# Kernel tuning notes

Measured on AMD Instinct MI355X. Metric: run time of the kernel, lower is better.

The kernel has to match this reference:

```python
import jax, jax.numpy as jnp
import numpy as np

B, IN_E, IN_I, D = 4096, 4096, 4096, 2048
IN_BR = 8192
BS = IN_BR // D  # block size = 4
K_E, K_I = 50, 1
E_TO_I = 50.0
BN_EPS = 1e-5


def setup_inputs() -> dict:
    key = jax.random.key(0)
    ks = jax.random.split(key, 8)
    # fan-in uniform init like nn.Linear (kaiming-uniform bound ~ 1/sqrt(in))
    def linw(k, out_f, in_f):
        b = 1.0 / np.sqrt(in_f)
        return jax.random.uniform(k, (out_f, in_f), jnp.float32, -b, b)
    return {
        "excitatory_input": jax.random.normal(ks[0], (B, IN_E), jnp.float32),
        "inhibitory_input": jax.random.normal(ks[1], (B, IN_I), jnp.float32),
        "dendrite_branch_outputs": jax.random.uniform(ks[2], (B, IN_BR), jnp.float32),
        "w_exc": linw(ks[3], D, IN_E),
        "w_inh": linw(ks[4], D, IN_I),
        "w_block": linw(ks[5], D, IN_BR),
        "bn_gamma": jnp.ones((D,), jnp.float32),
        "bn_beta": jnp.zeros((D,), jnp.float32),
    }


def _topk_linear(x, w, k):
    # keep the k largest weights per output row, zero the rest, then matmul
    idx = jax.lax.top_k(w, k)[1]                          # [D, k]
    mask = jnp.zeros_like(w).at[jnp.arange(w.shape[0])[:, None], idx].set(1.0)
    return x @ (w * mask).T                               # [B, D]


def _block_linear(x, w):
    # block-diagonal mask: row c uses columns [c*BS, (c+1)*BS)
    out_f = w.shape[0]
    wb = w.reshape(out_f, out_f, BS)[jnp.arange(out_f), jnp.arange(out_f)]  # [D, BS]
    xb = x.reshape(x.shape[0], out_f, BS)                                   # [B, D, BS]
    return jnp.einsum('bds,ds->bd', xb, wb)


def reference(excitatory_input, inhibitory_input, dendrite_branch_outputs,
              w_exc, w_inh, w_block, bn_gamma, bn_beta):
    dendrite_excitation = _topk_linear(excitatory_input, w_exc, K_E)
    dendrite_inhibition = _topk_linear(inhibitory_input, w_inh, K_I)
    dendrite_depolarization = _block_linear(dendrite_branch_outputs, w_block)
    total_excitatory = dendrite_excitation + dendrite_depolarization
    # neuron_type == 'excitatory'
    act = total_excitatory - E_TO_I * dendrite_inhibition
    # BatchNorm1d, training mode: batch stats, biased variance
    mean = jnp.mean(act, axis=0)
    var = jnp.var(act, axis=0)
    act = (act - mean) * jax.lax.rsqrt(var + BN_EPS) * bn_gamma + bn_beta
    return jax.nn.sigmoid(act)
```

## Files before the change

### kernel.cpp

```cpp
#include <hip/hip_runtime.h>
#include <hip/hip_fp16.h>

#define B_     4096
#define INE_   4096
#define INBR_  8192
#define D_     2048
#define KE_    50
#define KPAD_  52
#define CAP_   512

__device__ __forceinline__ unsigned packh2(float a, float b) {
  __half2 h = __floats2half2_rn(a, b);
  return __builtin_bit_cast(unsigned, h);
}
__device__ __forceinline__ float2 unpackh2(unsigned u) {
  __half2 h = __builtin_bit_cast(__half2, u);
  return __half22float2(h);
}

__global__ __launch_bounds__(256) void extract_diag(
    const float* __restrict__ wblock, float* __restrict__ wdiag)
{
  int d = blockIdx.x * 256 + threadIdx.x;
  float4 w = *reinterpret_cast<const float4*>(wblock + (size_t)d * (INBR_ + 4));
  reinterpret_cast<float4*>(wdiag)[d] = w;
}

__global__ __launch_bounds__(256) void topk_kernel(
    const float* __restrict__ W, int k, int kpad, float hi, float t0,
    float vscale, unsigned* __restrict__ out_off, float* __restrict__ out_val)
{
  const int row = blockIdx.x;
  const int t   = threadIdx.x;
  const float* wr = W + (size_t)row * INE_;

  __shared__ float cval[CAP_];
  __shared__ int   ccol[CAP_];
  __shared__ int   scnt;
  __shared__ int   red[4];

  float thr = t0;
  int M = 0;
  for (int attempt = 0; attempt < 8; ++attempt) {
    int local = 0;
    #pragma unroll
    for (int j = 0; j < 4; ++j) {
      float4 w4 = *reinterpret_cast<const float4*>(wr + 4 * (t + 256 * j));
      local += (w4.x > thr) + (w4.y > thr) + (w4.z > thr) + (w4.w > thr);
    }
    #pragma unroll
    for (int off = 32; off > 0; off >>= 1) local += __shfl_down(local, off);
    if ((t & 63) == 0) red[t >> 6] = local;
    __syncthreads();
    M = red[0] + red[1] + red[2] + red[3];
    __syncthreads();
    if (M >= k && M <= CAP_) break;
    if (M < k) thr = hi - (hi - thr) * 4.0f;
    else       thr = hi - (hi - thr) * 0.5f;
  }

  if (t == 0) scnt = 0;
  __syncthreads();
  #pragma unroll
  for (int j = 0; j < 4; ++j) {
    int cbase = 4 * (t + 256 * j);
    float4 w4 = *reinterpret_cast<const float4*>(wr + cbase);
    float wv[4] = {w4.x, w4.y, w4.z, w4.w};
    #pragma unroll
    for (int q = 0; q < 4; ++q) {
      if (wv[q] > thr) {
        int p = atomicAdd(&scnt, 1);
        if (p < CAP_) { cval[p] = wv[q]; ccol[p] = cbase + q; }
      }
    }
  }
  __syncthreads();
  M = scnt < CAP_ ? scnt : CAP_;

  for (int i = t; i < M; i += 256) {
    float wi = cval[i]; int ci = ccol[i];
    int rank = 0;
    for (int m = 0; m < M; ++m) {
      float wm = cval[m]; int cm = ccol[m];
      rank += (wm > wi || (wm == wi && cm < ci)) ? 1 : 0;
    }
    if (rank < k) {
      unsigned c = (unsigned)ci;
      unsigned off = ((c >> 2) << 3) | ((c & 3u) << 13);
      float    val = wi * vscale;
      if (kpad == 1) {
        out_off[row] = off;
        out_val[row] = val;
      } else {
        size_t idx = ((size_t)(rank >> 2) * D_ + row) * 4 + (rank & 3);
        out_off[idx] = off;
        out_val[idx] = val;
      }
    }
  }
  if (kpad > 1 && t < kpad - k) {
    int slot = k + t;
    size_t idx = ((size_t)(slot >> 2) * D_ + row) * 4 + (slot & 3);
    out_off[idx] = 0u;
    out_val[idx] = 0.0f;
  }
}

__device__ __forceinline__ void stage_rows4(const float* __restrict__ src,
                                            unsigned* xs, int b0, int p, int Q) {
  const float* r0p = src + (size_t)(b0 + 2 * p)     * INE_;
  const float* r1p = src + (size_t)(b0 + 2 * p + 1) * INE_;
  #pragma unroll
  for (int m = 0; m < 4; ++m) {
    int c0 = 4 * Q + 1024 * m;
    float4 fa = *reinterpret_cast<const float4*>(r0p + c0);
    float4 fb = *reinterpret_cast<const float4*>(r1p + c0);
    int wb = 2 * (Q + 256 * m) + p;
    xs[wb]        = packh2(fa.x, fb.x);
    xs[wb + 2048] = packh2(fa.y, fb.y);
    xs[wb + 4096] = packh2(fa.z, fb.z);
    xs[wb + 6144] = packh2(fa.w, fb.w);
  }
}

__device__ __forceinline__ uint2 ldg2(const char* ldsb, unsigned off) {
  return *reinterpret_cast<const uint2*>(ldsb + off);
}

#define FMA4(R, G, WV) do {                                                \
    float2 f0 = unpackh2((G).x), f1 = unpackh2((G).y);                     \
    acc[R][0] = fmaf(f0.x, (WV), acc[R][0]);                               \
    acc[R][1] = fmaf(f0.y, (WV), acc[R][1]);                               \
    acc[R][2] = fmaf(f1.x, (WV), acc[R][2]);                               \
    acc[R][3] = fmaf(f1.y, (WV), acc[R][3]);                               \
  } while (0)

__global__ __launch_bounds__(512, 4) void fused_main(
    const float* __restrict__ xe, const float* __restrict__ xi,
    const float* __restrict__ xbr, const float* __restrict__ wdiag,
    const unsigned* __restrict__ soT, const float* __restrict__ veT,
    const unsigned* __restrict__ so_inh, const float* __restrict__ vi_inh,
    float* __restrict__ act)
{
  __shared__ unsigned xs[8192];
  const int t  = threadIdx.x;
  const int b0 = blockIdx.x * 4;
  const int p  = t & 1;
  const int Q  = t >> 1;

  float acc[4][4];
  #pragma unroll
  for (int r = 0; r < 4; ++r)
    #pragma unroll
    for (int b = 0; b < 4; ++b) acc[r][b] = 0.0f;

  const char* ldsb = reinterpret_cast<const char*>(xs);
  const uint4*  soT4 = reinterpret_cast<const uint4*>(soT);
  const float4* veT4 = reinterpret_cast<const float4*>(veT);

  stage_rows4(xe, xs, b0, p, Q);
  __syncthreads();
  for (int ii = 0; ii < KPAD_ / 4; ++ii) {
    uint4 o[4]; float4 v[4];
    #pragma unroll
    for (int r = 0; r < 4; ++r) {
      o[r] = soT4[ii * D_ + t + 512 * r];
      v[r] = veT4[ii * D_ + t + 512 * r];
    }
    uint2 g[4][4];
    #pragma unroll
    for (int r = 0; r < 4; ++r) {
      g[r][0] = ldg2(ldsb, o[r].x);
      g[r][1] = ldg2(ldsb, o[r].y);
      g[r][2] = ldg2(ldsb, o[r].z);
      g[r][3] = ldg2(ldsb, o[r].w);
    }
    #pragma unroll
    for (int r = 0; r < 4; ++r) {
      FMA4(r, g[r][0], v[r].x);
      FMA4(r, g[r][1], v[r].y);
      FMA4(r, g[r][2], v[r].z);
      FMA4(r, g[r][3], v[r].w);
    }
  }
  __syncthreads();

  stage_rows4(xi, xs, b0, p, Q);
  unsigned oi[4]; float vi[4];
  #pragma unroll
  for (int r = 0; r < 4; ++r) {
    const int d = t + 512 * r;
    oi[r] = so_inh[d];
    vi[r] = vi_inh[d];
  }
  __syncthreads();
  {
    uint2 gi[4];
    #pragma unroll
    for (int r = 0; r < 4; ++r) gi[r] = ldg2(ldsb, oi[r]);
    #pragma unroll
    for (int r = 0; r < 4; ++r) FMA4(r, gi[r], vi[r]);
  }

  #pragma unroll
  for (int r = 0; r < 4; ++r) {
    const int d = t + 512 * r;
    float4 wb4 = reinterpret_cast<const float4*>(wdiag)[d];
    #pragma unroll
    for (int b = 0; b < 4; ++b) {
      float4 xb4 = *reinterpret_cast<const float4*>(
          xbr + (size_t)(b0 + b) * INBR_ + 4 * d);
      acc[r][b] += xb4.x * wb4.x + xb4.y * wb4.y + xb4.z * wb4.z + xb4.w * wb4.w;
    }
  }

  #pragma unroll
  for (int r = 0; r < 4; ++r) {
    const int d = t + 512 * r;
    #pragma unroll
    for (int b = 0; b < 4; ++b)
      act[(size_t)(b0 + b) * D_ + d] = acc[r][b];
  }
}

__global__ __launch_bounds__(256) void reduce_stats(
    const float* __restrict__ act, float* __restrict__ sums,
    float* __restrict__ sumsq)
{
  const int dg = blockIdx.x & 63;
  const int rg = blockIdx.x >> 6;
  const int tx = threadIdx.x & 31;
  const int ty = threadIdx.x >> 5;
  const int d  = dg * 32 + tx;

  float s = 0.0f, s2 = 0.0f;
  #pragma unroll 4
  for (int i = 0; i < 64; ++i) {
    int row = rg * 512 + ty + 8 * i;
    float a = act[(size_t)row * D_ + d];
    s += a;
    s2 = fmaf(a, a, s2);
  }
  __shared__ float ls[2][8][32];
  ls[0][ty][tx] = s;
  ls[1][ty][tx] = s2;
  __syncthreads();
  if (ty == 0) {
    #pragma unroll
    for (int j = 1; j < 8; ++j) { s += ls[0][j][tx]; s2 += ls[1][j][tx]; }
    atomicAdd(&sums[d], s);
    atomicAdd(&sumsq[d], s2);
  }
}

__global__ __launch_bounds__(256) void finalize_stats(
    const float* __restrict__ sums, const float* __restrict__ sumsq,
    const float* __restrict__ gamma, const float* __restrict__ beta,
    float* __restrict__ scsh)
{
  int d = blockIdx.x * 256 + threadIdx.x;
  if (d < D_) {
    float mean = sums[d]  * (1.0f / B_);
    float var  = sumsq[d] * (1.0f / B_) - mean * mean;
    float rstd = rsqrtf(var + 1e-5f);
    float sc   = gamma[d] * rstd;
    scsh[2 * d]     = sc;
    scsh[2 * d + 1] = fmaf(-mean, sc, beta[d]);
  }
}

__global__ __launch_bounds__(256) void norm_sigmoid(
    float* __restrict__ act, const float* __restrict__ scsh)
{
  const int total4 = (B_ * D_) / 4;
  for (int i = blockIdx.x * blockDim.x + threadIdx.x; i < total4;
       i += gridDim.x * blockDim.x) {
    float4 a = reinterpret_cast<float4*>(act)[i];
    int d0 = (i * 4) & (D_ - 1);
    const float4* sp = reinterpret_cast<const float4*>(scsh + 2 * d0);
    float4 s0 = sp[0];
    float4 s1 = sp[1];
    float z0 = fmaf(a.x, s0.x, s0.y);
    float z1 = fmaf(a.y, s0.z, s0.w);
    float z2 = fmaf(a.z, s1.x, s1.y);
    float z3 = fmaf(a.w, s1.z, s1.w);
    a.x = 1.0f / (1.0f + __expf(-z0));
    a.y = 1.0f / (1.0f + __expf(-z1));
    a.z = 1.0f / (1.0f + __expf(-z2));
    a.w = 1.0f / (1.0f + __expf(-z3));
    reinterpret_cast<float4*>(act)[i] = a;
  }
}

extern "C" void kernel_launch(void* const* d_in, const int* in_sizes, int n_in,
                              void* d_out, int out_size, void* d_ws, size_t ws_size,
                              hipStream_t stream) {
  const float* xe    = (const float*)d_in[0];
  const float* xi    = (const float*)d_in[1];
  const float* xbr   = (const float*)d_in[2];
  const float* wexc  = (const float*)d_in[3];
  const float* winh  = (const float*)d_in[4];
  const float* wblk  = (const float*)d_in[5];
  const float* gamma = (const float*)d_in[6];
  const float* beta  = (const float*)d_in[7];
  float* act = (float*)d_out;

  char* ws = (char*)d_ws;
  unsigned* soT    = (unsigned*)(ws + 0);
  float*    veT    = (float*)   (ws + 425984);
  unsigned* so_inh = (unsigned*)(ws + 851968);
  float*    vi_inh = (float*)   (ws + 860160);
  float*    wdiag  = (float*)   (ws + 868352);
  float*    sums   = (float*)   (ws + 901120);
  float*    sumsq  = (float*)   (ws + 909312);
  float*    scsh   = (float*)   (ws + 917504);

  hipMemsetAsync(sums, 0, 2 * D_ * sizeof(float), stream);

  const float hi = 0.015625f;
  extract_diag<<<dim3(8), dim3(256), 0, stream>>>(wblk, wdiag);
  topk_kernel<<<dim3(D_), dim3(256), 0, stream>>>(
      wexc, KE_, KPAD_, hi, hi * (1.0f - 200.0f / 4096.0f), 1.0f, soT, veT);
  topk_kernel<<<dim3(D_), dim3(256), 0, stream>>>(
      winh, 1, 1, hi, hi * (1.0f - 48.0f / 4096.0f), -50.0f, so_inh, vi_inh);
  fused_main<<<dim3(B_ / 4), dim3(512), 0, stream>>>(
      xe, xi, xbr, wdiag, soT, veT, so_inh, vi_inh, act);
  reduce_stats<<<dim3(512), dim3(256), 0, stream>>>(act, sums, sumsq);
  finalize_stats<<<dim3((D_ + 255) / 256), dim3(256), 0, stream>>>(
      sums, sumsq, gamma, beta, scsh);
  norm_sigmoid<<<dim3(2048), dim3(256), 0, stream>>>(act, scsh);
}
```

Baseline: 141.4 us.

## Merge prep kernels, fuse BN stats into main kernel, overlap loads with gather

The three preprocessing kernels (diagonal extraction and the two top-k selections) are merged into one launch. The main kernel now accumulates per-feature sum and sum-of-squares with atomics into four slice buffers, which removes the separate pass that re-read the activations. Inhibitory input rows and the block-diagonal branch terms are loaded while the excitatory gather loop runs, to hide global latency. Finalize and normalize+sigmoid are combined into one tail kernel that keeps the scale/shift table in shared memory. In exchange there is more atomic traffic and higher register pressure in the main kernel.

```diff
diff --git a/kernel.cpp b/kernel.cpp
--- a/kernel.cpp
+++ b/kernel.cpp
@@ -8,6 +8,7 @@
 #define KE_    50
 #define KPAD_  52
 #define CAP_   512
+#define NSL_   4
 
 __device__ __forceinline__ unsigned packh2(float a, float b) {
   __half2 h = __floats2half2_rn(a, b);
@@ -18,20 +19,11 @@
   return __half22float2(h);
 }
 
-__global__ __launch_bounds__(256) void extract_diag(
-    const float* __restrict__ wblock, float* __restrict__ wdiag)
+__device__ void topk_body(const float* __restrict__ W, int row, int k, int kpad,
+                          float hi, float t0, float vscale,
+                          unsigned* __restrict__ out_off, float* __restrict__ out_val)
 {
-  int d = blockIdx.x * 256 + threadIdx.x;
-  float4 w = *reinterpret_cast<const float4*>(wblock + (size_t)d * (INBR_ + 4));
-  reinterpret_cast<float4*>(wdiag)[d] = w;
-}
-
-__global__ __launch_bounds__(256) void topk_kernel(
-    const float* __restrict__ W, int k, int kpad, float hi, float t0,
-    float vscale, unsigned* __restrict__ out_off, float* __restrict__ out_val)
-{
-  const int row = blockIdx.x;
-  const int t   = threadIdx.x;
+  const int t = threadIdx.x;
   const float* wr = W + (size_t)row * INE_;
 
   __shared__ float cval[CAP_];
@@ -69,8 +61,8 @@
     #pragma unroll
     for (int q = 0; q < 4; ++q) {
       if (wv[q] > thr) {
-        int p = atomicAdd(&scnt, 1);
-        if (p < CAP_) { cval[p] = wv[q]; ccol[p] = cbase + q; }
+        int pp = atomicAdd(&scnt, 1);
+        if (pp < CAP_) { cval[pp] = wv[q]; ccol[pp] = cbase + q; }
       }
     }
   }
@@ -106,6 +98,32 @@
   }
 }
 
+__global__ __launch_bounds__(256) void prep_kernel(
+    const float* __restrict__ wexc, const float* __restrict__ winh,
+    const float* __restrict__ wblk,
+    unsigned* __restrict__ soT, float* __restrict__ veT,
+    unsigned* __restrict__ so_inh, float* __restrict__ vi_inh,
+    float* __restrict__ wdiag)
+{
+  const int bid = blockIdx.x;
+  const float hi = 0.015625f;
+  if (bid < 2048) {
+    topk_body(wexc, bid, KE_, KPAD_, hi, hi * (1.0f - 200.0f / 4096.0f), 1.0f,
+              soT, veT);
+  } else if (bid < 4096) {
+    topk_body(winh, bid - 2048, 1, 1, hi, hi * (1.0f - 48.0f / 4096.0f), -50.0f,
+              so_inh, vi_inh);
+  } else {
+    const int t = threadIdx.x;
+    #pragma unroll
+    for (int j = 0; j < 8; ++j) {
+      int d = t + 256 * j;
+      float4 w = *reinterpret_cast<const float4*>(wblk + (size_t)d * (INBR_ + 4));
+      reinterpret_cast<float4*>(wdiag)[d] = w;
+    }
+  }
+}
+
 __device__ __forceinline__ void stage_rows4(const float* __restrict__ src,
                                             unsigned* xs, int b0, int p, int Q) {
   const float* r0p = src + (size_t)(b0 + 2 * p)     * INE_;
@@ -135,12 +153,49 @@
     acc[R][3] = fmaf(f1.y, (WV), acc[R][3]);                               \
   } while (0)
 
+#define GATHER_ITER(II) do {                                               \
+    uint4 o_[4]; float4 v_[4];                                             \
+    _Pragma("unroll")                                                      \
+    for (int r = 0; r < 4; ++r) {                                          \
+      o_[r] = soT4[(II) * D_ + t + 512 * r];                               \
+      v_[r] = veT4[(II) * D_ + t + 512 * r];                               \
+    }                                                                      \
+    uint2 gq_[4][4];                                                       \
+    _Pragma("unroll")                                                      \
+    for (int r = 0; r < 4; ++r) {                                          \
+      gq_[r][0] = ldg2(ldsb, o_[r].x);                                     \
+      gq_[r][1] = ldg2(ldsb, o_[r].y);                                     \
+      gq_[r][2] = ldg2(ldsb, o_[r].z);                                     \
+      gq_[r][3] = ldg2(ldsb, o_[r].w);                                     \
+    }                                                                      \
+    _Pragma("unroll")                                                      \
+    for (int r = 0; r < 4; ++r) {                                          \
+      FMA4(r, gq_[r][0], v_[r].x);                                         \
+      FMA4(r, gq_[r][1], v_[r].y);                                         \
+      FMA4(r, gq_[r][2], v_[r].z);                                         \
+      FMA4(r, gq_[r][3], v_[r].w);                                         \
+    }                                                                      \
+  } while (0)
+
+#define BR_CHUNK(R_) do {                                                  \
+    const int d_ = t + 512 * (R_);                                         \
+    float4 wb4 = reinterpret_cast<const float4*>(wdiag)[d_];               \
+    _Pragma("unroll")                                                      \
+    for (int b = 0; b < 4; ++b) {                                          \
+      float4 xb4 = *reinterpret_cast<const float4*>(                       \
+          xbr + (size_t)(b0 + b) * INBR_ + 4 * d_);                        \
+      acc[R_][b] += xb4.x * wb4.x + xb4.y * wb4.y +                        \
+                    xb4.z * wb4.z + xb4.w * wb4.w;                         \
+    }                                                                      \
+  } while (0)
+
 __global__ __launch_bounds__(512, 4) void fused_main(
     const float* __restrict__ xe, const float* __restrict__ xi,
     const float* __restrict__ xbr, const float* __restrict__ wdiag,
     const unsigned* __restrict__ soT, const float* __restrict__ veT,
     const unsigned* __restrict__ so_inh, const float* __restrict__ vi_inh,
-    float* __restrict__ act)
+    float* __restrict__ act, float* __restrict__ sums_p,
+    float* __restrict__ sumsq_p)
 {
   __shared__ unsigned xs[8192];
   const int t  = threadIdx.x;
@@ -160,135 +215,114 @@
 
   stage_rows4(xe, xs, b0, p, Q);
   __syncthreads();
-  for (int ii = 0; ii < KPAD_ / 4; ++ii) {
-    uint4 o[4]; float4 v[4];
-    #pragma unroll
-    for (int r = 0; r < 4; ++r) {
-      o[r] = soT4[ii * D_ + t + 512 * r];
-      v[r] = veT4[ii * D_ + t + 512 * r];
-    }
-    uint2 g[4][4];
-    #pragma unroll
-    for (int r = 0; r < 4; ++r) {
-      g[r][0] = ldg2(ldsb, o[r].x);
-      g[r][1] = ldg2(ldsb, o[r].y);
-      g[r][2] = ldg2(ldsb, o[r].z);
-      g[r][3] = ldg2(ldsb, o[r].w);
-    }
-    #pragma unroll
-    for (int r = 0; r < 4; ++r) {
-      FMA4(r, g[r][0], v[r].x);
-      FMA4(r, g[r][1], v[r].y);
-      FMA4(r, g[r][2], v[r].z);
-      FMA4(r, g[r][3], v[r].w);
-    }
-  }
-  __syncthreads();
-
-  stage_rows4(xi, xs, b0, p, Q);
-  unsigned oi[4]; float vi[4];
+
+  float4 xia[4], xib[4];
+  {
+    const float* xr0 = xi + (size_t)(b0 + 2 * p)     * INE_;
+    const float* xr1 = xi + (size_t)(b0 + 2 * p + 1) * INE_;
+    #pragma unroll
+    for (int m = 0; m < 4; ++m) {
+      xia[m] = *reinterpret_cast<const float4*>(xr0 + 4 * Q + 1024 * m);
+      xib[m] = *reinterpret_cast<const float4*>(xr1 + 4 * Q + 1024 * m);
+    }
+  }
+  unsigned oi[4]; float viv[4];
+  #pragma unroll
+  for (int r = 0; r < 4; ++r) {
+    oi[r]  = so_inh[t + 512 * r];
+    viv[r] = vi_inh[t + 512 * r];
+  }
+
+  #pragma unroll
+  for (int g = 0; g < 4; ++g) {
+    for (int jj = 0; jj < 3; ++jj) {
+      int ii = 3 * g + jj;
+      GATHER_ITER(ii);
+    }
+    BR_CHUNK(g);
+  }
+  GATHER_ITER(12);
+  __syncthreads();
+
+  #pragma unroll
+  for (int m = 0; m < 4; ++m) {
+    int wb = 2 * (Q + 256 * m) + p;
+    xs[wb]        = packh2(xia[m].x, xib[m].x);
+    xs[wb + 2048] = packh2(xia[m].y, xib[m].y);
+    xs[wb + 4096] = packh2(xia[m].z, xib[m].z);
+    xs[wb + 6144] = packh2(xia[m].w, xib[m].w);
+  }
+  __syncthreads();
+  {
+    uint2 gi[4];
+    #pragma unroll
+    for (int r = 0; r < 4; ++r) gi[r] = ldg2(ldsb, oi[r]);
+    #pragma unroll
+    for (int r = 0; r < 4; ++r) FMA4(r, gi[r], viv[r]);
+  }
+
+  const int slice = blockIdx.x >> 8;
   #pragma unroll
   for (int r = 0; r < 4; ++r) {
     const int d = t + 512 * r;
-    oi[r] = so_inh[d];
-    vi[r] = vi_inh[d];
-  }
-  __syncthreads();
-  {
-    uint2 gi[4];
-    #pragma unroll
-    for (int r = 0; r < 4; ++r) gi[r] = ldg2(ldsb, oi[r]);
-    #pragma unroll
-    for (int r = 0; r < 4; ++r) FMA4(r, gi[r], vi[r]);
-  }
-
-  #pragma unroll
-  for (int r = 0; r < 4; ++r) {
-    const int d = t + 512 * r;
-    float4 wb4 = reinterpret_cast<const float4*>(wdiag)[d];
+    float s = 0.0f, s2 = 0.0f;
     #pragma unroll
     for (int b = 0; b < 4; ++b) {
-      float4 xb4 = *reinterpret_cast<const float4*>(
-          xbr + (size_t)(b0 + b) * INBR_ + 4 * d);
-      acc[r][b] += xb4.x * wb4.x + xb4.y * wb4.y + xb4.z * wb4.z + xb4.w * wb4.w;
-    }
-  }
-
-  #pragma unroll
-  for (int r = 0; r < 4; ++r) {
-    const int d = t + 512 * r;
-    #pragma unroll
-    for (int b = 0; b < 4; ++b)
-      act[(size_t)(b0 + b) * D_ + d] = acc[r][b];
-  }
-}
-
-__global__ __launch_bounds__(256) void reduce_stats(
-    const float* __restrict__ act, float* __restrict__ sums,
-    float* __restrict__ sumsq)
+      float a = acc[r][b];
+      act[(size_t)(b0 + b) * D_ + d] = a;
+      s += a;
+      s2 = fmaf(a, a, s2);
+    }
+    atomicAdd(&sums_p[slice * D_ + d], s);
+    atomicAdd(&sumsq_p[slice * D_ + d], s2);
+  }
+}
+
+__global__ __launch_bounds__(256) void tail_kernel(
+    float* __restrict__ act, const float* __restrict__ sums_p,
+    const float* __restrict__ sumsq_p, const float* __restrict__ gamma,
+    const float* __restrict__ beta)
 {
-  const int dg = blockIdx.x & 63;
-  const int rg = blockIdx.x >> 6;
-  const int tx = threadIdx.x & 31;
-  const int ty = threadIdx.x >> 5;
-  const int d  = dg * 32 + tx;
-
-  float s = 0.0f, s2 = 0.0f;
-  #pragma unroll 4
-  for (int i = 0; i < 64; ++i) {
-    int row = rg * 512 + ty + 8 * i;
-    float a = act[(size_t)row * D_ + d];
-    s += a;
-    s2 = fmaf(a, a, s2);
-  }
-  __shared__ float ls[2][8][32];
-  ls[0][ty][tx] = s;
-  ls[1][ty][tx] = s2;
-  __syncthreads();
-  if (ty == 0) {
-    #pragma unroll
-    for (int j = 1; j < 8; ++j) { s += ls[0][j][tx]; s2 += ls[1][j][tx]; }
-    atomicAdd(&sums[d], s);
-    atomicAdd(&sumsq[d], s2);
-  }
-}
-
-__global__ __launch_bounds__(256) void finalize_stats(
-    const float* __restrict__ sums, const float* __restrict__ sumsq,
-    const float* __restrict__ gamma, const float* __restrict__ beta,
-    float* __restrict__ scsh)
-{
-  int d = blockIdx.x * 256 + threadIdx.x;
-  if (d < D_) {
-    float mean = sums[d]  * (1.0f / B_);
-    float var  = sumsq[d] * (1.0f / B_) - mean * mean;
+  __shared__ float scsh[2 * D_];
+  const int tid = threadIdx.x;
+  #pragma unroll
+  for (int j = 0; j < 8; ++j) {
+    int d = tid + 256 * j;
+    float s = 0.0f, s2 = 0.0f;
+    #pragma unroll
+    for (int sl = 0; sl < NSL_; ++sl) {
+      s  += sums_p[sl * D_ + d];
+      s2 += sumsq_p[sl * D_ + d];
+    }
+    float mean = s  * (1.0f / B_);
+    float var  = s2 * (1.0f / B_) - mean * mean;
     float rstd = rsqrtf(var + 1e-5f);
     float sc   = gamma[d] * rstd;
     scsh[2 * d]     = sc;
     scsh[2 * d + 1] = fmaf(-mean, sc, beta[d]);
   }
-}
-
-__global__ __launch_bounds__(256) void norm_sigmoid(
-    float* __restrict__ act, const float* __restrict__ scsh)
-{
-  const int total4 = (B_ * D_) / 4;
-  for (int i = blockIdx.x * blockDim.x + threadIdx.x; i < total4;
-       i += gridDim.x * blockDim.x) {
-    float4 a = reinterpret_cast<float4*>(act)[i];
-    int d0 = (i * 4) & (D_ - 1);
-    const float4* sp = reinterpret_cast<const float4*>(scsh + 2 * d0);
-    float4 s0 = sp[0];
-    float4 s1 = sp[1];
-    float z0 = fmaf(a.x, s0.x, s0.y);
-    float z1 = fmaf(a.y, s0.z, s0.w);
-    float z2 = fmaf(a.z, s1.x, s1.y);
-    float z3 = fmaf(a.w, s1.z, s1.w);
-    a.x = 1.0f / (1.0f + __expf(-z0));
-    a.y = 1.0f / (1.0f + __expf(-z1));
-    a.z = 1.0f / (1.0f + __expf(-z2));
-    a.w = 1.0f / (1.0f + __expf(-z3));
-    reinterpret_cast<float4*>(act)[i] = a;
+  __syncthreads();
+
+  const int r0 = blockIdx.x * 8;
+  for (int rr = 0; rr < 8; ++rr) {
+    float4* rowp = reinterpret_cast<float4*>(act + (size_t)(r0 + rr) * D_);
+    #pragma unroll
+    for (int i2 = 0; i2 < 2; ++i2) {
+      int i = tid + 256 * i2;
+      float4 a = rowp[i];
+      const float4* sp = reinterpret_cast<const float4*>(scsh + 8 * i);
+      float4 s0 = sp[0];
+      float4 s1 = sp[1];
+      float z0 = fmaf(a.x, s0.x, s0.y);
+      float z1 = fmaf(a.y, s0.z, s0.w);
+      float z2 = fmaf(a.z, s1.x, s1.y);
+      float z3 = fmaf(a.w, s1.z, s1.w);
+      a.x = 1.0f / (1.0f + __expf(-z0));
+      a.y = 1.0f / (1.0f + __expf(-z1));
+      a.z = 1.0f / (1.0f + __expf(-z2));
+      a.w = 1.0f / (1.0f + __expf(-z3));
+      rowp[i] = a;
+    }
   }
 }
 
@@ -306,27 +340,20 @@
   float* act = (float*)d_out;
 
   char* ws = (char*)d_ws;
-  unsigned* soT    = (unsigned*)(ws + 0);
-  float*    veT    = (float*)   (ws + 425984);
-  unsigned* so_inh = (unsigned*)(ws + 851968);
-  float*    vi_inh = (float*)   (ws + 860160);
-  float*    wdiag  = (float*)   (ws + 868352);
-  float*    sums   = (float*)   (ws + 901120);
-  float*    sumsq  = (float*)   (ws + 909312);
-  float*    scsh   = (float*)   (ws + 917504);
-
-  hipMemsetAsync(sums, 0, 2 * D_ * sizeof(float), stream);
-
-  const float hi = 0.015625f;
-  extract_diag<<<dim3(8), dim3(256), 0, stream>>>(wblk, wdiag);
-  topk_kernel<<<dim3(D_), dim3(256), 0, stream>>>(
-      wexc, KE_, KPAD_, hi, hi * (1.0f - 200.0f / 4096.0f), 1.0f, soT, veT);
-  topk_kernel<<<dim3(D_), dim3(256), 0, stream>>>(
-      winh, 1, 1, hi, hi * (1.0f - 48.0f / 4096.0f), -50.0f, so_inh, vi_inh);
+  unsigned* soT     = (unsigned*)(ws + 0);
+  float*    veT     = (float*)   (ws + 425984);
+  unsigned* so_inh  = (unsigned*)(ws + 851968);
+  float*    vi_inh  = (float*)   (ws + 860160);
+  float*    wdiag   = (float*)   (ws + 868352);
+  float*    sums_p  = (float*)   (ws + 901120);
+  float*    sumsq_p = (float*)   (ws + 933888);
+
+  hipMemsetAsync(sums_p, 0, 2 * NSL_ * D_ * sizeof(float), stream);
+
+  prep_kernel<<<dim3(4097), dim3(256), 0, stream>>>(
+      wexc, winh, wblk, soT, veT, so_inh, vi_inh, wdiag);
   fused_main<<<dim3(B_ / 4), dim3(512), 0, stream>>>(
-      xe, xi, xbr, wdiag, soT, veT, so_inh, vi_inh, act);
-  reduce_stats<<<dim3(512), dim3(256), 0, stream>>>(act, sums, sumsq);
-  finalize_stats<<<dim3((D_ + 255) / 256), dim3(256), 0, stream>>>(
-      sums, sumsq, gamma, beta, scsh);
-  norm_sigmoid<<<dim3(2048), dim3(256), 0, stream>>>(act, scsh);
-}
+      xe, xi, xbr, wdiag, soT, veT, so_inh, vi_inh, act, sums_p, sumsq_p);
+  tail_kernel<<<dim3(512), dim3(256), 0, stream>>>(
+      act, sums_p, sumsq_p, gamma, beta);
+}
```

After: 150.1 us. 1.06x slower.

## Split branch term into separate blocks, merge prep and tail kernels

Applied to the files above, without the earlier changes.

Combines the diag extraction and both top-k selections into one prep launch. The main kernel now interleaves two roles across blocks: gather-FMA blocks for the excitatory/inhibitory terms and streaming blocks for the block-diagonal branch term. These write to separate workspace buffers, and the launch bound allows higher occupancy. Finalize and normalize+sigmoid are fused into one tail kernel that sums the two partial buffers. The cost is an extra 32 MB activation buffer that must be written and then read twice.

```diff
diff --git a/kernel.cpp b/kernel.cpp
--- a/kernel.cpp
+++ b/kernel.cpp
@@ -18,20 +18,11 @@
   return __half22float2(h);
 }
 
-__global__ __launch_bounds__(256) void extract_diag(
-    const float* __restrict__ wblock, float* __restrict__ wdiag)
-{
-  int d = blockIdx.x * 256 + threadIdx.x;
-  float4 w = *reinterpret_cast<const float4*>(wblock + (size_t)d * (INBR_ + 4));
-  reinterpret_cast<float4*>(wdiag)[d] = w;
-}
-
-__global__ __launch_bounds__(256) void topk_kernel(
-    const float* __restrict__ W, int k, int kpad, float hi, float t0,
-    float vscale, unsigned* __restrict__ out_off, float* __restrict__ out_val)
-{
-  const int row = blockIdx.x;
-  const int t   = threadIdx.x;
+__device__ void topk_body(const float* __restrict__ W, int row, int k, int kpad,
+                          float hi, float t0, float vscale,
+                          unsigned* __restrict__ out_off, float* __restrict__ out_val)
+{
+  const int t = threadIdx.x;
   const float* wr = W + (size_t)row * INE_;
 
   __shared__ float cval[CAP_];
@@ -69,8 +60,8 @@
     #pragma unroll
     for (int q = 0; q < 4; ++q) {
       if (wv[q] > thr) {
-        int p = atomicAdd(&scnt, 1);
-        if (p < CAP_) { cval[p] = wv[q]; ccol[p] = cbase + q; }
+        int pp = atomicAdd(&scnt, 1);
+        if (pp < CAP_) { cval[pp] = wv[q]; ccol[pp] = cbase + q; }
       }
     }
   }
@@ -106,6 +97,32 @@
   }
 }
 
+__global__ __launch_bounds__(256) void prep_kernel(
+    const float* __restrict__ wexc, const float* __restrict__ winh,
+    const float* __restrict__ wblk,
+    unsigned* __restrict__ soT, float* __restrict__ veT,
+    unsigned* __restrict__ so_inh, float* __restrict__ vi_inh,
+    float* __restrict__ wdiag)
+{
+  const int bid = blockIdx.x;
+  const float hi = 0.015625f;
+  if (bid < 2048) {
+    topk_body(wexc, bid, KE_, KPAD_, hi, hi * (1.0f - 200.0f / 4096.0f), 1.0f,
+              soT, veT);
+  } else if (bid < 4096) {
+    topk_body(winh, bid - 2048, 1, 1, hi, hi * (1.0f - 48.0f / 4096.0f), -50.0f,
+              so_inh, vi_inh);
+  } else {
+    const int t = threadIdx.x;
+    #pragma unroll
+    for (int j = 0; j < 8; ++j) {
+      int d = t + 256 * j;
+      float4 w = *reinterpret_cast<const float4*>(wblk + (size_t)d * (INBR_ + 4));
+      reinterpret_cast<float4*>(wdiag)[d] = w;
+    }
+  }
+}
+
 __device__ __forceinline__ void stage_rows4(const float* __restrict__ src,
                                             unsigned* xs, int b0, int p, int Q) {
   const float* r0p = src + (size_t)(b0 + 2 * p)     * INE_;
@@ -135,16 +152,16 @@
     acc[R][3] = fmaf(f1.y, (WV), acc[R][3]);                               \
   } while (0)
 
-__global__ __launch_bounds__(512, 4) void fused_main(
-    const float* __restrict__ xe, const float* __restrict__ xi,
-    const float* __restrict__ xbr, const float* __restrict__ wdiag,
-    const unsigned* __restrict__ soT, const float* __restrict__ veT,
-    const unsigned* __restrict__ so_inh, const float* __restrict__ vi_inh,
-    float* __restrict__ act)
-{
-  __shared__ unsigned xs[8192];
+__device__ void ei_role(int kb, const float* __restrict__ xe,
+                        const float* __restrict__ xi,
+                        const unsigned* __restrict__ soT,
+                        const float* __restrict__ veT,
+                        const unsigned* __restrict__ so_inh,
+                        const float* __restrict__ vi_inh,
+                        float* __restrict__ actE, unsigned* xs)
+{
   const int t  = threadIdx.x;
-  const int b0 = blockIdx.x * 4;
+  const int b0 = kb * 4;
   const int p  = t & 1;
   const int Q  = t >> 1;
 
@@ -186,46 +203,79 @@
   __syncthreads();
 
   stage_rows4(xi, xs, b0, p, Q);
-  unsigned oi[4]; float vi[4];
+  unsigned oi[4]; float viv[4];
+  #pragma unroll
+  for (int r = 0; r < 4; ++r) {
+    oi[r]  = so_inh[t + 512 * r];
+    viv[r] = vi_inh[t + 512 * r];
+  }
+  __syncthreads();
+  {
+    uint2 gi[4];
+    #pragma unroll
+    for (int r = 0; r < 4; ++r) gi[r] = ldg2(ldsb, oi[r]);
+    #pragma unroll
+    for (int r = 0; r < 4; ++r) FMA4(r, gi[r], viv[r]);
+  }
+
   #pragma unroll
   for (int r = 0; r < 4; ++r) {
     const int d = t + 512 * r;
-    oi[r] = so_inh[d];
-    vi[r] = vi_inh[d];
-  }
-  __syncthreads();
-  {
-    uint2 gi[4];
-    #pragma unroll
-    for (int r = 0; r < 4; ++r) gi[r] = ldg2(ldsb, oi[r]);
-    #pragma unroll
-    for (int r = 0; r < 4; ++r) FMA4(r, gi[r], vi[r]);
-  }
-
-  #pragma unroll
-  for (int r = 0; r < 4; ++r) {
-    const int d = t + 512 * r;
-    float4 wb4 = reinterpret_cast<const float4*>(wdiag)[d];
-    #pragma unroll
-    for (int b = 0; b < 4; ++b) {
-      float4 xb4 = *reinterpret_cast<const float4*>(
-          xbr + (size_t)(b0 + b) * INBR_ + 4 * d);
-      acc[r][b] += xb4.x * wb4.x + xb4.y * wb4.y + xb4.z * wb4.z + xb4.w * wb4.w;
-    }
-  }
-
-  #pragma unroll
-  for (int r = 0; r < 4; ++r) {
-    const int d = t + 512 * r;
     #pragma unroll
     for (int b = 0; b < 4; ++b)
-      act[(size_t)(b0 + b) * D_ + d] = acc[r][b];
-  }
-}
-
-__global__ __launch_bounds__(256) void reduce_stats(
-    const float* __restrict__ act, float* __restrict__ sums,
-    float* __restrict__ sumsq)
+      actE[(size_t)(b0 + b) * D_ + d] = acc[r][b];
+  }
+}
+
+__device__ void br_role(int kb, const float* __restrict__ xbr,
+                        const float* __restrict__ wdiag,
+                        float* __restrict__ actBR)
+{
+  const int t = threadIdx.x;
+  const float4* xbr4 = reinterpret_cast<const float4*>(xbr);
+  const float4* wd4  = reinterpret_cast<const float4*>(wdiag);
+  float4*       out4 = reinterpret_cast<float4*>(actBR);
+
+  float4 w0 = wd4[4 * t], w1 = wd4[4 * t + 1],
+         w2 = wd4[4 * t + 2], w3 = wd4[4 * t + 3];
+  #pragma unroll
+  for (int rr = 0; rr < 8; ++rr) {
+    int row = 8 * kb + rr;
+    const float4* xp = xbr4 + (size_t)row * (INBR_ / 4) + 4 * t;
+    float4 x0 = xp[0], x1 = xp[1], x2 = xp[2], x3 = xp[3];
+    float4 a;
+    a.x = x0.x * w0.x + x0.y * w0.y + x0.z * w0.z + x0.w * w0.w;
+    a.y = x1.x * w1.x + x1.y * w1.y + x1.z * w1.z + x1.w * w1.w;
+    a.z = x2.x * w2.x + x2.y * w2.y + x2.z * w2.z + x2.w * w2.w;
+    a.w = x3.x * w3.x + x3.y * w3.y + x3.z * w3.z + x3.w * w3.w;
+    out4[(size_t)row * (D_ / 4) + t] = a;
+  }
+}
+
+__global__ __launch_bounds__(512, 8) void mega_kernel(
+    const float* __restrict__ xe, const float* __restrict__ xi,
+    const float* __restrict__ xbr, const float* __restrict__ wdiag,
+    const unsigned* __restrict__ soT, const float* __restrict__ veT,
+    const unsigned* __restrict__ so_inh, const float* __restrict__ vi_inh,
+    float* __restrict__ actE, float* __restrict__ actBR)
+{
+  __shared__ unsigned xs[8192];
+  const int i = blockIdx.x;
+  const int g = i & 7;
+  const int j = i >> 3;
+  const int m3 = j % 3;
+  if (m3 < 2) {
+    int kb = ((j / 3) * 2 + m3) * 8 + g;
+    ei_role(kb, xe, xi, soT, veT, so_inh, vi_inh, actE, xs);
+  } else {
+    int kb = (j / 3) * 8 + g;
+    br_role(kb, xbr, wdiag, actBR);
+  }
+}
+
+__global__ __launch_bounds__(256) void reduce_stats2(
+    const float* __restrict__ actE, const float* __restrict__ actBR,
+    float* __restrict__ sums, float* __restrict__ sumsq)
 {
   const int dg = blockIdx.x & 63;
   const int rg = blockIdx.x >> 6;
@@ -237,7 +287,8 @@
   #pragma unroll 4
   for (int i = 0; i < 64; ++i) {
     int row = rg * 512 + ty + 8 * i;
-    float a = act[(size_t)row * D_ + d];
+    size_t idx = (size_t)row * D_ + d;
+    float a = actE[idx] + actBR[idx];
     s += a;
     s2 = fmaf(a, a, s2);
   }
@@ -247,19 +298,23 @@
   __syncthreads();
   if (ty == 0) {
     #pragma unroll
-    for (int j = 1; j < 8; ++j) { s += ls[0][j][tx]; s2 += ls[1][j][tx]; }
+    for (int jj = 1; jj < 8; ++jj) { s += ls[0][jj][tx]; s2 += ls[1][jj][tx]; }
     atomicAdd(&sums[d], s);
     atomicAdd(&sumsq[d], s2);
   }
 }
 
-__global__ __launch_bounds__(256) void finalize_stats(
-    const float* __restrict__ sums, const float* __restrict__ sumsq,
-    const float* __restrict__ gamma, const float* __restrict__ beta,
-    float* __restrict__ scsh)
-{
-  int d = blockIdx.x * 256 + threadIdx.x;
-  if (d < D_) {
+__global__ __launch_bounds__(256) void tail_kernel2(
+    const float* __restrict__ actE, const float* __restrict__ actBR,
+    float* __restrict__ out, const float* __restrict__ sums,
+    const float* __restrict__ sumsq, const float* __restrict__ gamma,
+    const float* __restrict__ beta)
+{
+  __shared__ float scsh[2 * D_];
+  const int tid = threadIdx.x;
+  #pragma unroll
+  for (int j = 0; j < 8; ++j) {
+    int d = tid + 256 * j;
     float mean = sums[d]  * (1.0f / B_);
     float var  = sumsq[d] * (1.0f / B_) - mean * mean;
     float rstd = rsqrtf(var + 1e-5f);
@@ -267,28 +322,32 @@
     scsh[2 * d]     = sc;
     scsh[2 * d + 1] = fmaf(-mean, sc, beta[d]);
   }
-}
-
-__global__ __launch_bounds__(256) void norm_sigmoid(
-    float* __restrict__ act, const float* __restrict__ scsh)
-{
-  const int total4 = (B_ * D_) / 4;
-  for (int i = blockIdx.x * blockDim.x + threadIdx.x; i < total4;
-       i += gridDim.x * blockDim.x) {
-    float4 a = reinterpret_cast<float4*>(act)[i];
-    int d0 = (i * 4) & (D_ - 1);
-    const float4* sp = reinterpret_cast<const float4*>(scsh + 2 * d0);
-    float4 s0 = sp[0];
-    float4 s1 = sp[1];
-    float z0 = fmaf(a.x, s0.x, s0.y);
-    float z1 = fmaf(a.y, s0.z, s0.w);
-    float z2 = fmaf(a.z, s1.x, s1.y);
-    float z3 = fmaf(a.w, s1.z, s1.w);
-    a.x = 1.0f / (1.0f + __expf(-z0));
-    a.y = 1.0f / (1.0f + __expf(-z1));
-    a.z = 1.0f / (1.0f + __expf(-z2));
-    a.w = 1.0f / (1.0f + __expf(-z3));
-    reinterpret_cast<float4*>(act)[i] = a;
+  __syncthreads();
+
+  const int r0 = blockIdx.x * 8;
+  for (int rr = 0; rr < 8; ++rr) {
+    const float4* ep = reinterpret_cast<const float4*>(actE  + (size_t)(r0 + rr) * D_);
+    const float4* bp = reinterpret_cast<const float4*>(actBR + (size_t)(r0 + rr) * D_);
+    float4*       op = reinterpret_cast<float4*>(out + (size_t)(r0 + rr) * D_);
+    #pragma unroll
+    for (int i2 = 0; i2 < 2; ++i2) {
+      int i = tid + 256 * i2;
+      float4 e = ep[i];
+      float4 b = bp[i];
+      const float4* sp = reinterpret_cast<const float4*>(scsh + 8 * i);
+      float4 s0 = sp[0];
+      float4 s1 = sp[1];
+      float z0 = fmaf(e.x + b.x, s0.x, s0.y);
+      float z1 = fmaf(e.y + b.y, s0.z, s0.w);
+      float z2 = fmaf(e.z + b.z, s1.x, s1.y);
+      float z3 = fmaf(e.w + b.w, s1.z, s1.w);
+      float4 a;
+      a.x = 1.0f / (1.0f + __expf(-z0));
+      a.y = 1.0f / (1.0f + __expf(-z1));
+      a.z = 1.0f / (1.0f + __expf(-z2));
+      a.w = 1.0f / (1.0f + __expf(-z3));
+      op[i] = a;
+    }
   }
 }
 
@@ -303,7 +362,7 @@
   const float* wblk  = (const float*)d_in[5];
   const float* gamma = (const float*)d_in[6];
   const float* beta  = (const float*)d_in[7];
-  float* act = (float*)d_out;
+  float* out = (float*)d_out;
 
   char* ws = (char*)d_ws;
   unsigned* soT    = (unsigned*)(ws + 0);
@@ -313,20 +372,16 @@
   float*    wdiag  = (float*)   (ws + 868352);
   float*    sums   = (float*)   (ws + 901120);
   float*    sumsq  = (float*)   (ws + 909312);
-  float*    scsh   = (float*)   (ws + 917504);
+  float*    actE   = (float*)   (ws + 1048576);
+  float*    actBR  = (float*)   (ws + 34603008);
 
   hipMemsetAsync(sums, 0, 2 * D_ * sizeof(float), stream);
 
-  const float hi = 0.015625f;
-  extract_diag<<<dim3(8), dim3(256), 0, stream>>>(wblk, wdiag);
-  topk_kernel<<<dim3(D_), dim3(256), 0, stream>>>(
-      wexc, KE_, KPAD_, hi, hi * (1.0f - 200.0f / 4096.0f), 1.0f, soT, veT);
-  topk_kernel<<<dim3(D_), dim3(256), 0, stream>>>(
-      winh, 1, 1, hi, hi * (1.0f - 48.0f / 4096.0f), -50.0f, so_inh, vi_inh);
-  fused_main<<<dim3(B_ / 4), dim3(512), 0, stream>>>(
-      xe, xi, xbr, wdiag, soT, veT, so_inh, vi_inh, act);
-  reduce_stats<<<dim3(512), dim3(256), 0, stream>>>(act, sums, sumsq);
-  finalize_stats<<<dim3((D_ + 255) / 256), dim3(256), 0, stream>>>(
-      sums, sumsq, gamma, beta, scsh);
-  norm_sigmoid<<<dim3(2048), dim3(256), 0, stream>>>(act, scsh);
-}
+  prep_kernel<<<dim3(4097), dim3(256), 0, stream>>>(
+      wexc, winh, wblk, soT, veT, so_inh, vi_inh, wdiag);
+  mega_kernel<<<dim3(1536), dim3(512), 0, stream>>>(
+      xe, xi, xbr, wdiag, soT, veT, so_inh, vi_inh, actE, actBR);
+  reduce_stats2<<<dim3(512), dim3(256), 0, stream>>>(actE, actBR, sums, sumsq);
+  tail_kernel2<<<dim3(512), dim3(256), 0, stream>>>(
+      actE, actBR, out, sums, sumsq, gamma, beta);
+}
```

Result: slower. 168.2 us (+19.0%).
